# Optimization experiments

Hardware: AMD Instinct MI355X
Metric: run time of the kernel (lower is better)

The kernel has to match this reference:

```python
import jax, jax.numpy as jnp
import numpy as np

N_HEAD = 16
D_MODEL = 1024
D_HEAD = D_MODEL // N_HEAD
B, T = 2, 2048


def setup_inputs() -> dict:
    key = jax.random.key(0)
    k1, k2, k3 = jax.random.split(key, 3)
    x = jax.random.normal(k1, (B, T, D_MODEL), dtype=jnp.float32)
    w_attn = jax.random.normal(k2, (3 * D_MODEL, D_MODEL), dtype=jnp.float32) * (D_MODEL ** -0.5)
    w_proj = jax.random.normal(k3, (D_MODEL, D_MODEL), dtype=jnp.float32) * (D_MODEL ** -0.5)
    return {"x": x, "w_attn": w_attn, "w_proj": w_proj}


def _rms_norm(x):
    eps = jnp.asarray(jnp.finfo(x.dtype).eps, x.dtype)
    var = jnp.mean(jnp.square(x), axis=-1, keepdims=True)
    return x * jax.lax.rsqrt(var + eps)


def _rotate_half(x):
    x1, x2 = jnp.split(x, 2, axis=-1)
    return jnp.concatenate((-x2, x1), axis=-1)


def reference(x, w_attn, w_proj):
    Bx, Tx, C = x.shape
    qkv = jnp.einsum('btc,fc->btf', x, w_attn)  # [B,T,3C]
    q, k, v = jnp.split(qkv, 3, axis=-1)
    # [B, H, T, Dh]
    q = q.reshape(Bx, Tx, N_HEAD, D_HEAD).transpose(0, 2, 1, 3)
    k = k.reshape(Bx, Tx, N_HEAD, D_HEAD).transpose(0, 2, 1, 3)
    v = v.reshape(Bx, Tx, N_HEAD, D_HEAD).transpose(0, 2, 1, 3)
    # QK RMSNorm (no learned weight)
    q = _rms_norm(q)
    k = _rms_norm(k)
    # Rotary embedding over full d_head: freqs tiled twice
    inv_freq = 1.0 / (10000.0 ** (jnp.arange(0, D_HEAD, 2, dtype=jnp.float32) / D_HEAD))
    t = jnp.arange(Tx, dtype=jnp.float32)
    freqs = jnp.einsum('i,j->ij', t, inv_freq)  # [T, Dh/2]
    emb = jnp.concatenate((freqs, freqs), axis=-1)  # [T, Dh]
    cos = jnp.cos(emb)[None, None, :, :]
    sin = jnp.sin(emb)[None, None, :, :]
    q = q * cos + _rotate_half(q) * sin
    k = k * cos + _rotate_half(k) * sin
    # Causal SDPA
    scale = D_HEAD ** -0.5
    scores = jnp.einsum('bhqd,bhkd->bhqk', q, k) * scale
    causal = jnp.tril(jnp.ones((Tx, Tx), dtype=bool))
    scores = jnp.where(causal[None, None], scores, jnp.asarray(-jnp.inf, scores.dtype))
    attn = jax.nn.softmax(scores, axis=-1)
    y = jnp.einsum('bhqk,bhkd->bhqd', attn, v)
    y = y.transpose(0, 2, 1, 3).reshape(Bx, Tx, C)
    return jnp.einsum('btc,oc->bto', y, w_proj)
```

## Files before the change

kernel.cpp:

```cpp
#include <hip/hip_runtime.h>
#include <cstdint>
#include <cstddef>


typedef short bf16x8 __attribute__((ext_vector_type(8)));
typedef float floatx4 __attribute__((ext_vector_type(4)));
typedef unsigned short ushortx8 __attribute__((ext_vector_type(8)));
typedef unsigned short ushortx4 __attribute__((ext_vector_type(4)));

#define DEVI __device__ __forceinline__

DEVI float bf2f(unsigned short u) {
    unsigned int x = ((unsigned int)u) << 16;
    return __builtin_bit_cast(float, x);
}
DEVI unsigned short f2bf(float f) {
    unsigned int u = __builtin_bit_cast(unsigned int, f);
    u += 0x7fffu + ((u >> 16) & 1u);
    return (unsigned short)(u >> 16);
}

DEVI void glds16(const unsigned short* g, unsigned short* l) {
    __builtin_amdgcn_global_load_lds(
        (const __attribute__((address_space(1))) unsigned int*)g,
        (__attribute__((address_space(3))) unsigned int*)l, 16, 0, 0);
}

DEVI void cast8(unsigned short* dst, const float* src) {
    floatx4 a = *(const floatx4*)src;
    floatx4 b = *(const floatx4*)(src + 4);
    ushortx8 o;
    o[0] = f2bf(a[0]); o[1] = f2bf(a[1]); o[2] = f2bf(a[2]); o[3] = f2bf(a[3]);
    o[4] = f2bf(b[0]); o[5] = f2bf(b[1]); o[6] = f2bf(b[2]); o[7] = f2bf(b[3]);
    *(ushortx8*)dst = o;
}

__global__ __launch_bounds__(256)
void cast_inputs(const float* __restrict__ x, const float* __restrict__ wa,
                 const float* __restrict__ wp,
                 unsigned short* __restrict__ xb, unsigned short* __restrict__ wab,
                 unsigned short* __restrict__ wpb)
{
    size_t g = (size_t)blockIdx.x * 256 + threadIdx.x;
    size_t stride = (size_t)gridDim.x * 256;
    for (size_t i = g; i < (4194304 / 8); i += stride) cast8(xb  + i * 8, x  + i * 8);
    for (size_t i = g; i < (3145728 / 8); i += stride) cast8(wab + i * 8, wa + i * 8);
    for (size_t i = g; i < (1048576 / 8); i += stride) cast8(wpb + i * 8, wp + i * 8);
}

template <bool QKV_SPLIT>
__global__ __launch_bounds__(256)
void gemm_bt(const unsigned short* __restrict__ A, const unsigned short* __restrict__ B,
             unsigned short* __restrict__ Cqk, float* __restrict__ Cf,
             unsigned short* __restrict__ Vt, int M, int N, int K)
{
    __shared__ __align__(16) unsigned short As[128 * 32];
    __shared__ __align__(16) unsigned short Bs[128 * 32];

    const int tid  = threadIdx.x;
    const int lane = tid & 63;
    const int w    = tid >> 6;
    const int wm   = w >> 1, wn = w & 1;
    const int quad = lane >> 4;
    const int lm   = lane & 15;
    const int m0 = blockIdx.y * 128;
    const int n0 = blockIdx.x * 128;
    const int sr = lane >> 2;
    const int sc = (lane & 3) * 8;

    floatx4 acc[4][4] = {};

    for (int k0 = 0; k0 < K; k0 += 32) {
        __syncthreads();
        #pragma unroll
        for (int i = 0; i < 2; ++i) {
            int r = w * 32 + i * 16;
            glds16(&A[(size_t)(m0 + r + sr) * K + k0 + sc], &As[r * 32]);
            glds16(&B[(size_t)(n0 + r + sr) * K + k0 + sc], &Bs[r * 32]);
        }
        __syncthreads();

        bf16x8 a[4];
        #pragma unroll
        for (int i = 0; i < 4; ++i)
            a[i] = *(const bf16x8*)&As[(wm * 64 + i * 16 + lm) * 32 + quad * 8];
        #pragma unroll
        for (int j = 0; j < 4; ++j) {
            bf16x8 b = *(const bf16x8*)&Bs[(wn * 64 + j * 16 + lm) * 32 + quad * 8];
            #pragma unroll
            for (int i = 0; i < 4; ++i)
                acc[i][j] = __builtin_amdgcn_mfma_f32_16x16x32_bf16(a[i], b, acc[i][j], 0, 0, 0);
        }
    }

    #pragma unroll
    for (int i = 0; i < 4; ++i) {
        #pragma unroll
        for (int j = 0; j < 4; ++j) {
            int col = n0 + wn * 64 + j * 16 + lm;
            #pragma unroll
            for (int r = 0; r < 4; ++r) {
                int row = m0 + wm * 64 + i * 16 + quad * 4 + r;
                if constexpr (QKV_SPLIT) {
                    unsigned short v = f2bf(acc[i][j][r]);
                    if (col < 2048) {
                        Cqk[(size_t)row * 2048 + col] = v;
                    } else {
                        int bq = row >> 11, t = row & 2047;
                        Vt[((size_t)(bq * 1024 + (col - 2048))) * 2048 + t] = v;
                    }
                } else {
                    Cf[(size_t)row * N + col] = acc[i][j][r];
                }
            }
        }
    }
}

__global__ __launch_bounds__(256)
void rmsnorm_rope(unsigned short* __restrict__ qk)
{
    int gw   = (blockIdx.x * 256 + threadIdx.x) >> 6;
    int lane = threadIdx.x & 63;
    int h = gw & 15;
    int t = (gw >> 4) & 2047;
    int b = gw >> 15;

    size_t base = ((size_t)(b * 2048 + t)) * 2048 + h * 64 + lane;
    float q = bf2f(qk[base]);
    float k = bf2f(qk[base + 1024]);

    float sq = q * q, sk = k * k;
    #pragma unroll
    for (int off = 32; off >= 1; off >>= 1) {
        sq += __shfl_xor(sq, off, 64);
        sk += __shfl_xor(sk, off, 64);
    }
    const float eps = 1.1920929e-07f;
    q *= rsqrtf(sq * (1.0f / 64.0f) + eps);
    k *= rsqrtf(sk * (1.0f / 64.0f) + eps);

    int i = lane & 31;
    float ang = (float)t * expf(-(float)i * 0.28782313662425572f);
    float c = cosf(ang), s = sinf(ang);
    float qp = __shfl_xor(q, 32, 64);
    float kp = __shfl_xor(k, 32, 64);
    float sgn = (lane < 32) ? -1.0f : 1.0f;
    float qo = q * c + sgn * qp * s;
    float ko = k * c + sgn * kp * s;

    qk[base]        = f2bf(qo);
    qk[base + 1024] = f2bf(ko);
}

__global__ __launch_bounds__(256)
void attention(const unsigned short* __restrict__ qk,
               const unsigned short* __restrict__ Vt,
               unsigned short* __restrict__ Y)
{
    constexpr int LD = 72;
    __shared__ __align__(16) unsigned short QPs[64 * LD];
    __shared__ __align__(16) unsigned short Ks [64 * LD];
    __shared__ __align__(16) unsigned short Vs [64 * LD];

    const int tid  = threadIdx.x;
    const int lane = tid & 63;
    const int w    = tid >> 6;
    const int quad = lane >> 4;
    const int lm   = lane & 15;

    const int bh = blockIdx.x;
    const int qt = 31 - blockIdx.y;
    const int b  = bh >> 4, h = bh & 15;
    const int q0 = qt * 64;
    const int qrow = q0 + w * 16 + lm;

    #pragma unroll
    for (int i = 0; i < 2; ++i) {
        int c = i * 256 + tid, row = c >> 3, col = (c & 7) * 8;
        *(ushortx8*)&QPs[row * LD + col] =
            *(const ushortx8*)&qk[((size_t)(b * 2048 + q0 + row)) * 2048 + h * 64 + col];
    }

    ushortx8 kreg[2], vreg[2];
    #pragma unroll
    for (int i = 0; i < 2; ++i) {
        int c = i * 256 + tid, row = c >> 3, col = (c & 7) * 8;
        kreg[i] = *(const ushortx8*)&qk[((size_t)(b * 2048 + row)) * 2048 + 1024 + h * 64 + col];
        vreg[i] = *(const ushortx8*)&Vt[((size_t)(bh * 64 + row)) * 2048 + col];
    }

    floatx4 o[4] = {};
    float lsum = 0.0f;
    bf16x8 qf[2];
    const float c1 = 0.125f * 1.44269504f;
    const float c2 = 8.0f   * 1.44269504f;

    for (int kt = 0; kt <= qt; ++kt) {
        const int k0 = kt * 64;
        __syncthreads();
        #pragma unroll
        for (int i = 0; i < 2; ++i) {
            int c = i * 256 + tid, row = c >> 3, col = (c & 7) * 8;
            *(ushortx8*)&Ks[row * LD + col] = kreg[i];
            *(ushortx8*)&Vs[row * LD + col] = vreg[i];
        }
        __syncthreads();

        if (kt == 0) {
            #pragma unroll
            for (int kk = 0; kk < 2; ++kk)
                qf[kk] = *(const bf16x8*)&QPs[(w * 16 + lm) * LD + kk * 32 + quad * 8];
        }
        if (kt < qt) {
            const int kn = k0 + 64;
            #pragma unroll
            for (int i = 0; i < 2; ++i) {
                int c = i * 256 + tid, row = c >> 3, col = (c & 7) * 8;
                kreg[i] = *(const ushortx8*)&qk[((size_t)(b * 2048 + kn + row)) * 2048 + 1024 + h * 64 + col];
                vreg[i] = *(const ushortx8*)&Vt[((size_t)(bh * 64 + row)) * 2048 + kn + col];
            }
        }

        floatx4 sa[4] = {};
        #pragma unroll
        for (int kk = 0; kk < 2; ++kk) {
            #pragma unroll
            for (int j = 0; j < 4; ++j) {
                bf16x8 kf = *(const bf16x8*)&Ks[(j * 16 + lm) * LD + kk * 32 + quad * 8];
                sa[j] = __builtin_amdgcn_mfma_f32_16x16x32_bf16(kf, qf[kk], sa[j], 0, 0, 0);
            }
        }

        const bool dg = (kt == qt);
        #pragma unroll
        for (int j = 0; j < 4; ++j) {
            int kbase = k0 + j * 16 + quad * 4;
            ushortx4 pk;
            #pragma unroll
            for (int r = 0; r < 4; ++r) {
                float p = exp2f(sa[j][r] * c1 - c2);
                if (dg && (kbase + r) > qrow) p = 0.0f;
                lsum += p;
                pk[r] = f2bf(p);
            }
            *(ushortx4*)&QPs[(w * 16 + lm) * LD + j * 16 + quad * 4] = pk;
        }

        #pragma unroll
        for (int kk = 0; kk < 2; ++kk) {
            bf16x8 pf = *(const bf16x8*)&QPs[(w * 16 + lm) * LD + kk * 32 + quad * 8];
            #pragma unroll
            for (int j = 0; j < 4; ++j) {
                bf16x8 vf = *(const bf16x8*)&Vs[(j * 16 + lm) * LD + kk * 32 + quad * 8];
                o[j] = __builtin_amdgcn_mfma_f32_16x16x32_bf16(pf, vf, o[j], 0, 0, 0);
            }
        }
    }

    float lt = lsum;
    lt += __shfl_xor(lt, 16, 64);
    lt += __shfl_xor(lt, 32, 64);
    float rv = 1.0f / lt;
    float rinv[4];
    #pragma unroll
    for (int r = 0; r < 4; ++r)
        rinv[r] = __shfl(rv, (quad << 4) + quad * 4 + r, 64);

    #pragma unroll
    for (int j = 0; j < 4; ++j) {
        int colg = h * 64 + j * 16 + lm;
        #pragma unroll
        for (int r = 0; r < 4; ++r) {
            int rowg = q0 + w * 16 + quad * 4 + r;
            Y[((size_t)(b * 2048 + rowg)) * 1024 + colg] = f2bf(o[j][r] * rinv[r]);
        }
    }
}

extern "C" void kernel_launch(void* const* d_in, const int* in_sizes, int n_in,
                              void* d_out, int out_size, void* d_ws, size_t ws_size,
                              hipStream_t stream)
{
    const float* x      = (const float*)d_in[0];
    const float* w_attn = (const float*)d_in[1];
    const float* w_proj = (const float*)d_in[2];
    float* out = (float*)d_out;

    unsigned short* qkbuf = (unsigned short*)d_ws;
    unsigned short* Vtb   = qkbuf + (size_t)4096 * 2048;
    unsigned short* y     = Vtb   + (size_t)32 * 64 * 2048;
    unsigned short* wpb   = y     + (size_t)4096 * 1024;
    unsigned short* xb  = (unsigned short*)d_out;
    unsigned short* wab = xb + (size_t)4096 * 1024;

    dim3 blk(256);
    cast_inputs<<<dim3(1024), blk, 0, stream>>>(x, w_attn, w_proj, xb, wab, wpb);
    gemm_bt<true>
        <<<dim3(24, 32), blk, 0, stream>>>(xb, wab, qkbuf, nullptr, Vtb, 4096, 3072, 1024);
    rmsnorm_rope<<<dim3(16384), blk, 0, stream>>>(qkbuf);
    attention<<<dim3(32, 32), blk, 0, stream>>>(qkbuf, Vtb, y);
    gemm_bt<false>
        <<<dim3(8, 32), blk, 0, stream>>>(y, wpb, nullptr, out, nullptr, 4096, 1024, 1024);
}
```

Baseline: 212.0 us.

## Double-buffer K/V register prefetch two tiles ahead and pack bf16 with perm

K/V tiles are now prefetched into a two-deep register ring, loading the tile two iterations ahead instead of one, so global-load latency has more compute to hide behind. The __syncthreads pairs are replaced by an inline-asm waitcnt lgkmcnt(0)+s_barrier. P conversion to bf16 now uses round-half-up plus a byte permute that packs two values per instruction, instead of round-to-nearest-even per element. The cost is more VGPRs for the extra prefetch buffers, which may lower occupancy, plus a slightly different bf16 rounding.

Result: slower. 719.7 us (+239.5%).

```diff
diff --git a/kernel.cpp b/kernel.cpp
--- a/kernel.cpp
+++ b/kernel.cpp
@@ -6,7 +6,7 @@
 typedef short bf16x8 __attribute__((ext_vector_type(8)));
 typedef float floatx4 __attribute__((ext_vector_type(4)));
 typedef unsigned short ushortx8 __attribute__((ext_vector_type(8)));
-typedef unsigned short ushortx4 __attribute__((ext_vector_type(4)));
+typedef unsigned int uintx2 __attribute__((ext_vector_type(2)));
 
 #define DEVI __device__ __forceinline__
 
@@ -18,6 +18,14 @@
     unsigned int u = __builtin_bit_cast(unsigned int, f);
     u += 0x7fffu + ((u >> 16) & 1u);
     return (unsigned short)(u >> 16);
+}
+DEVI unsigned int pkbf2(float a, float b) {
+    unsigned int ua = __builtin_bit_cast(unsigned int, a) + 0x8000u;
+    unsigned int ub = __builtin_bit_cast(unsigned int, b) + 0x8000u;
+    return __builtin_amdgcn_perm(ub, ua, 0x07060302);
+}
+DEVI void barrier_lgkm() {
+    asm volatile("s_waitcnt lgkmcnt(0)\ns_barrier" ::: "memory");
 }
 
 DEVI void glds16(const unsigned short* g, unsigned short* l) {
@@ -175,6 +183,11 @@
     const int q0 = qt * 64;
     const int qrow = q0 + w * 16 + lm;
 
+    const int pr0 = tid >> 3,        pc = (tid & 7) * 8;
+    const int pr1 = (256 + tid) >> 3;
+    const unsigned short* kbase = qk + (size_t)b * 2048 * 2048 + 1024 + h * 64;
+    const unsigned short* vbase = Vt + (size_t)bh * 64 * 2048;
+
     #pragma unroll
     for (int i = 0; i < 2; ++i) {
         int c = i * 256 + tid, row = c >> 3, col = (c & 7) * 8;
@@ -182,12 +195,17 @@
             *(const ushortx8*)&qk[((size_t)(b * 2048 + q0 + row)) * 2048 + h * 64 + col];
     }
 
-    ushortx8 kreg[2], vreg[2];
-    #pragma unroll
-    for (int i = 0; i < 2; ++i) {
-        int c = i * 256 + tid, row = c >> 3, col = (c & 7) * 8;
-        kreg[i] = *(const ushortx8*)&qk[((size_t)(b * 2048 + row)) * 2048 + 1024 + h * 64 + col];
-        vreg[i] = *(const ushortx8*)&Vt[((size_t)(bh * 64 + row)) * 2048 + col];
+    ushortx8 kreg[2][2], vreg[2][2];
+    {
+        kreg[0][0] = *(const ushortx8*)&kbase[(size_t)pr0 * 2048 + pc];
+        kreg[0][1] = *(const ushortx8*)&kbase[(size_t)pr1 * 2048 + pc];
+        vreg[0][0] = *(const ushortx8*)&vbase[(size_t)pr0 * 2048 + pc];
+        vreg[0][1] = *(const ushortx8*)&vbase[(size_t)pr1 * 2048 + pc];
+        int t1 = (qt >= 1) ? 64 : 0;
+        kreg[1][0] = *(const ushortx8*)&kbase[(size_t)(t1 + pr0) * 2048 + pc];
+        kreg[1][1] = *(const ushortx8*)&kbase[(size_t)(t1 + pr1) * 2048 + pc];
+        vreg[1][0] = *(const ushortx8*)&vbase[(size_t)pr0 * 2048 + t1 + pc];
+        vreg[1][1] = *(const ushortx8*)&vbase[(size_t)pr1 * 2048 + t1 + pc];
     }
 
     floatx4 o[4] = {};
@@ -198,28 +216,25 @@
 
     for (int kt = 0; kt <= qt; ++kt) {
         const int k0 = kt * 64;
-        __syncthreads();
-        #pragma unroll
-        for (int i = 0; i < 2; ++i) {
-            int c = i * 256 + tid, row = c >> 3, col = (c & 7) * 8;
-            *(ushortx8*)&Ks[row * LD + col] = kreg[i];
-            *(ushortx8*)&Vs[row * LD + col] = vreg[i];
-        }
-        __syncthreads();
+        const int cur = kt & 1;
+        barrier_lgkm();
+        *(ushortx8*)&Ks[pr0 * LD + pc] = kreg[cur][0];
+        *(ushortx8*)&Ks[pr1 * LD + pc] = kreg[cur][1];
+        *(ushortx8*)&Vs[pr0 * LD + pc] = vreg[cur][0];
+        *(ushortx8*)&Vs[pr1 * LD + pc] = vreg[cur][1];
+        barrier_lgkm();
 
         if (kt == 0) {
             #pragma unroll
             for (int kk = 0; kk < 2; ++kk)
                 qf[kk] = *(const bf16x8*)&QPs[(w * 16 + lm) * LD + kk * 32 + quad * 8];
         }
-        if (kt < qt) {
-            const int kn = k0 + 64;
-            #pragma unroll
-            for (int i = 0; i < 2; ++i) {
-                int c = i * 256 + tid, row = c >> 3, col = (c & 7) * 8;
-                kreg[i] = *(const ushortx8*)&qk[((size_t)(b * 2048 + kn + row)) * 2048 + 1024 + h * 64 + col];
-                vreg[i] = *(const ushortx8*)&Vt[((size_t)(bh * 64 + row)) * 2048 + kn + col];
-            }
+        if (kt + 2 <= qt) {
+            const int kn = k0 + 128;
+            kreg[cur][0] = *(const ushortx8*)&kbase[(size_t)(kn + pr0) * 2048 + pc];
+            kreg[cur][1] = *(const ushortx8*)&kbase[(size_t)(kn + pr1) * 2048 + pc];
+            vreg[cur][0] = *(const ushortx8*)&vbase[(size_t)pr0 * 2048 + kn + pc];
+            vreg[cur][1] = *(const ushortx8*)&vbase[(size_t)pr1 * 2048 + kn + pc];
         }
 
         floatx4 sa[4] = {};
@@ -235,16 +250,22 @@
         const bool dg = (kt == qt);
         #pragma unroll
         for (int j = 0; j < 4; ++j) {
-            int kbase = k0 + j * 16 + quad * 4;
-            ushortx4 pk;
-            #pragma unroll
-            for (int r = 0; r < 4; ++r) {
-                float p = exp2f(sa[j][r] * c1 - c2);
-                if (dg && (kbase + r) > qrow) p = 0.0f;
-                lsum += p;
-                pk[r] = f2bf(p);
+            int kb = k0 + j * 16 + quad * 4;
+            float p0 = exp2f(sa[j][0] * c1 - c2);
+            float p1 = exp2f(sa[j][1] * c1 - c2);
+            float p2 = exp2f(sa[j][2] * c1 - c2);
+            float p3 = exp2f(sa[j][3] * c1 - c2);
+            if (dg) {
+                if (kb + 0 > qrow) p0 = 0.0f;
+                if (kb + 1 > qrow) p1 = 0.0f;
+                if (kb + 2 > qrow) p2 = 0.0f;
+                if (kb + 3 > qrow) p3 = 0.0f;
             }
-            *(ushortx4*)&QPs[(w * 16 + lm) * LD + j * 16 + quad * 4] = pk;
+            lsum += (p0 + p1) + (p2 + p3);
+            uintx2 pk;
+            pk[0] = pkbf2(p0, p1);
+            pk[1] = pkbf2(p2, p3);
+            *(uintx2*)&QPs[(w * 16 + lm) * LD + j * 16 + quad * 4] = pk;
         }
 
         #pragma unroll
```

## Pair causal query tiles per attention block and narrow output-projection GEMM tiles

Applied to the files above, without the earlier changes.

The attention kernel now launches half as many blocks. Each block processes two query tiles, qt and 31-qt, so every block does the same total causal work instead of the triangular imbalance. The output-projection GEMM is templated to a 128x64 tile with a 4x1 wave layout, doubling its grid from 256 to 512 blocks to fill more CUs. In exchange, attention gets fewer concurrent blocks and runs longer serial loops per block, and the narrower GEMM tile reduces reuse of the A operand.

Result: no change. 209.5 us (-1.2%).

```diff
diff --git a/kernel.cpp b/kernel.cpp
--- a/kernel.cpp
+++ b/kernel.cpp
@@ -48,27 +48,31 @@
     for (size_t i = g; i < (1048576 / 8); i += stride) cast8(wpb + i * 8, wp + i * 8);
 }
 
-template <bool QKV_SPLIT>
+template <bool QKV_SPLIT, int BN>
 __global__ __launch_bounds__(256)
 void gemm_bt(const unsigned short* __restrict__ A, const unsigned short* __restrict__ B,
              unsigned short* __restrict__ Cqk, float* __restrict__ Cf,
              unsigned short* __restrict__ Vt, int M, int N, int K)
 {
+    constexpr int WCOLS = (BN == 128) ? 2 : 1;
+    constexpr int WROWS = 4 / WCOLS;
+    constexpr int MI    = 128 / (16 * WROWS);
+
     __shared__ __align__(16) unsigned short As[128 * 32];
-    __shared__ __align__(16) unsigned short Bs[128 * 32];
+    __shared__ __align__(16) unsigned short Bs[BN * 32];
 
     const int tid  = threadIdx.x;
     const int lane = tid & 63;
     const int w    = tid >> 6;
-    const int wm   = w >> 1, wn = w & 1;
+    const int wm   = w / WCOLS, wn = w % WCOLS;
     const int quad = lane >> 4;
     const int lm   = lane & 15;
     const int m0 = blockIdx.y * 128;
-    const int n0 = blockIdx.x * 128;
+    const int n0 = blockIdx.x * BN;
     const int sr = lane >> 2;
     const int sc = (lane & 3) * 8;
 
-    floatx4 acc[4][4] = {};
+    floatx4 acc[MI][4] = {};
 
     for (int k0 = 0; k0 < K; k0 += 32) {
         __syncthreads();
@@ -76,31 +80,35 @@
         for (int i = 0; i < 2; ++i) {
             int r = w * 32 + i * 16;
             glds16(&A[(size_t)(m0 + r + sr) * K + k0 + sc], &As[r * 32]);
+        }
+        #pragma unroll
+        for (int i = 0; i < BN / 64; ++i) {
+            int r = w * (BN / 4) + i * 16;
             glds16(&B[(size_t)(n0 + r + sr) * K + k0 + sc], &Bs[r * 32]);
         }
         __syncthreads();
 
-        bf16x8 a[4];
-        #pragma unroll
-        for (int i = 0; i < 4; ++i)
-            a[i] = *(const bf16x8*)&As[(wm * 64 + i * 16 + lm) * 32 + quad * 8];
+        bf16x8 a[MI];
+        #pragma unroll
+        for (int i = 0; i < MI; ++i)
+            a[i] = *(const bf16x8*)&As[(wm * (16 * MI) + i * 16 + lm) * 32 + quad * 8];
         #pragma unroll
         for (int j = 0; j < 4; ++j) {
             bf16x8 b = *(const bf16x8*)&Bs[(wn * 64 + j * 16 + lm) * 32 + quad * 8];
             #pragma unroll
-            for (int i = 0; i < 4; ++i)
+            for (int i = 0; i < MI; ++i)
                 acc[i][j] = __builtin_amdgcn_mfma_f32_16x16x32_bf16(a[i], b, acc[i][j], 0, 0, 0);
         }
     }
 
     #pragma unroll
-    for (int i = 0; i < 4; ++i) {
+    for (int i = 0; i < MI; ++i) {
         #pragma unroll
         for (int j = 0; j < 4; ++j) {
             int col = n0 + wn * 64 + j * 16 + lm;
             #pragma unroll
             for (int r = 0; r < 4; ++r) {
-                int row = m0 + wm * 64 + i * 16 + quad * 4 + r;
+                int row = m0 + wm * (16 * MI) + i * 16 + quad * 4 + r;
                 if constexpr (QKV_SPLIT) {
                     unsigned short v = f2bf(acc[i][j][r]);
                     if (col < 2048) {
@@ -170,110 +178,119 @@
     const int lm   = lane & 15;
 
     const int bh = blockIdx.x;
-    const int qt = 31 - blockIdx.y;
     const int b  = bh >> 4, h = bh & 15;
-    const int q0 = qt * 64;
-    const int qrow = q0 + w * 16 + lm;
+
+    const unsigned short* kbase = qk + (size_t)b * 2048 * 2048 + 1024 + h * 64;
+    const unsigned short* vbase = Vt + (size_t)bh * 64 * 2048;
 
     #pragma unroll
-    for (int i = 0; i < 2; ++i) {
-        int c = i * 256 + tid, row = c >> 3, col = (c & 7) * 8;
-        *(ushortx8*)&QPs[row * LD + col] =
-            *(const ushortx8*)&qk[((size_t)(b * 2048 + q0 + row)) * 2048 + h * 64 + col];
-    }
-
-    ushortx8 kreg[2], vreg[2];
-    #pragma unroll
-    for (int i = 0; i < 2; ++i) {
-        int c = i * 256 + tid, row = c >> 3, col = (c & 7) * 8;
-        kreg[i] = *(const ushortx8*)&qk[((size_t)(b * 2048 + row)) * 2048 + 1024 + h * 64 + col];
-        vreg[i] = *(const ushortx8*)&Vt[((size_t)(bh * 64 + row)) * 2048 + col];
-    }
-
-    floatx4 o[4] = {};
-    float lsum = 0.0f;
-    bf16x8 qf[2];
-    const float c1 = 0.125f * 1.44269504f;
-    const float c2 = 8.0f   * 1.44269504f;
-
-    for (int kt = 0; kt <= qt; ++kt) {
-        const int k0 = kt * 64;
-        __syncthreads();
+    for (int sel = 0; sel < 2; ++sel) {
+        const int qt = sel ? (int)blockIdx.y : 31 - (int)blockIdx.y;
+        const int q0 = qt * 64;
+        const int qrow = q0 + w * 16 + lm;
+
+        if (sel) __syncthreads();
+
         #pragma unroll
         for (int i = 0; i < 2; ++i) {
             int c = i * 256 + tid, row = c >> 3, col = (c & 7) * 8;
-            *(ushortx8*)&Ks[row * LD + col] = kreg[i];
-            *(ushortx8*)&Vs[row * LD + col] = vreg[i];
-        }
-        __syncthreads();
-
-        if (kt == 0) {
-            #pragma unroll
-            for (int kk = 0; kk < 2; ++kk)
-                qf[kk] = *(const bf16x8*)&QPs[(w * 16 + lm) * LD + kk * 32 + quad * 8];
-        }
-        if (kt < qt) {
-            const int kn = k0 + 64;
+            *(ushortx8*)&QPs[row * LD + col] =
+                *(const ushortx8*)&qk[((size_t)(b * 2048 + q0 + row)) * 2048 + h * 64 + col];
+        }
+
+        ushortx8 kreg[2], vreg[2];
+        #pragma unroll
+        for (int i = 0; i < 2; ++i) {
+            int c = i * 256 + tid, row = c >> 3, col = (c & 7) * 8;
+            kreg[i] = *(const ushortx8*)&kbase[(size_t)row * 2048 + col];
+            vreg[i] = *(const ushortx8*)&vbase[(size_t)row * 2048 + col];
+        }
+
+        floatx4 o[4] = {};
+        float lsum = 0.0f;
+        bf16x8 qf[2];
+        const float c1 = 0.125f * 1.44269504f;
+        const float c2 = 8.0f   * 1.44269504f;
+
+        for (int kt = 0; kt <= qt; ++kt) {
+            const int k0 = kt * 64;
+            __syncthreads();
             #pragma unroll
             for (int i = 0; i < 2; ++i) {
                 int c = i * 256 + tid, row = c >> 3, col = (c & 7) * 8;
-                kreg[i] = *(const ushortx8*)&qk[((size_t)(b * 2048 + kn + row)) * 2048 + 1024 + h * 64 + col];
-                vreg[i] = *(const ushortx8*)&Vt[((size_t)(bh * 64 + row)) * 2048 + kn + col];
-            }
-        }
-
-        floatx4 sa[4] = {};
-        #pragma unroll
-        for (int kk = 0; kk < 2; ++kk) {
+                *(ushortx8*)&Ks[row * LD + col] = kreg[i];
+                *(ushortx8*)&Vs[row * LD + col] = vreg[i];
+            }
+            __syncthreads();
+
+            if (kt == 0) {
+                #pragma unroll
+                for (int kk = 0; kk < 2; ++kk)
+                    qf[kk] = *(const bf16x8*)&QPs[(w * 16 + lm) * LD + kk * 32 + quad * 8];
+            }
+            if (kt < qt) {
+                const int kn = k0 + 64;
+                #pragma unroll
+                for (int i = 0; i < 2; ++i) {
+                    int c = i * 256 + tid, row = c >> 3, col = (c & 7) * 8;
+                    kreg[i] = *(const ushortx8*)&kbase[(size_t)(kn + row) * 2048 + col];
+                    vreg[i] = *(const ushortx8*)&vbase[(size_t)row * 2048 + kn + col];
+                }
+            }
+
+            floatx4 sa[4] = {};
+            #pragma unroll
+            for (int kk = 0; kk < 2; ++kk) {
+                #pragma unroll
+                for (int j = 0; j < 4; ++j) {
+                    bf16x8 kf = *(const bf16x8*)&Ks[(j * 16 + lm) * LD + kk * 32 + quad * 8];
+                    sa[j] = __builtin_amdgcn_mfma_f32_16x16x32_bf16(kf, qf[kk], sa[j], 0, 0, 0);
+                }
+            }
+
+            const bool dg = (kt == qt);
             #pragma unroll
             for (int j = 0; j < 4; ++j) {
-                bf16x8 kf = *(const bf16x8*)&Ks[(j * 16 + lm) * LD + kk * 32 + quad * 8];
-                sa[j] = __builtin_amdgcn_mfma_f32_16x16x32_bf16(kf, qf[kk], sa[j], 0, 0, 0);
-            }
-        }
-
-        const bool dg = (kt == qt);
+                int kb = k0 + j * 16 + quad * 4;
+                ushortx4 pk;
+                #pragma unroll
+                for (int r = 0; r < 4; ++r) {
+                    float p = exp2f(sa[j][r] * c1 - c2);
+                    if (dg && (kb + r) > qrow) p = 0.0f;
+                    lsum += p;
+                    pk[r] = f2bf(p);
+                }
+                *(ushortx4*)&QPs[(w * 16 + lm) * LD + j * 16 + quad * 4] = pk;
+            }
+
+            #pragma unroll
+            for (int kk = 0; kk < 2; ++kk) {
+                bf16x8 pf = *(const bf16x8*)&QPs[(w * 16 + lm) * LD + kk * 32 + quad * 8];
+                #pragma unroll
+                for (int j = 0; j < 4; ++j) {
+                    bf16x8 vf = *(const bf16x8*)&Vs[(j * 16 + lm) * LD + kk * 32 + quad * 8];
+                    o[j] = __builtin_amdgcn_mfma_f32_16x16x32_bf16(pf, vf, o[j], 0, 0, 0);
+                }
+            }
+        }
+
+        float lt = lsum;
+        lt += __shfl_xor(lt, 16, 64);
+        lt += __shfl_xor(lt, 32, 64);
+        float rv = 1.0f / lt;
+        float rinv[4];
+        #pragma unroll
+        for (int r = 0; r < 4; ++r)
+            rinv[r] = __shfl(rv, (quad << 4) + quad * 4 + r, 64);
+
         #pragma unroll
         for (int j = 0; j < 4; ++j) {
-            int kbase = k0 + j * 16 + quad * 4;
-            ushortx4 pk;
+            int colg = h * 64 + j * 16 + lm;
             #pragma unroll
             for (int r = 0; r < 4; ++r) {
-                float p = exp2f(sa[j][r] * c1 - c2);
-                if (dg && (kbase + r) > qrow) p = 0.0f;
-                lsum += p;
-                pk[r] = f2bf(p);
-            }
-            *(ushortx4*)&QPs[(w * 16 + lm) * LD + j * 16 + quad * 4] = pk;
-        }
-
-        #pragma unroll
-        for (int kk = 0; kk < 2; ++kk) {
-            bf16x8 pf = *(const bf16x8*)&QPs[(w * 16 + lm) * LD + kk * 32 + quad * 8];
-            #pragma unroll
-            for (int j = 0; j < 4; ++j) {
-                bf16x8 vf = *(const bf16x8*)&Vs[(j * 16 + lm) * LD + kk * 32 + quad * 8];
-                o[j] = __builtin_amdgcn_mfma_f32_16x16x32_bf16(pf, vf, o[j], 0, 0, 0);
-            }
-        }
-    }
-
-    float lt = lsum;
-    lt += __shfl_xor(lt, 16, 64);
-    lt += __shfl_xor(lt, 32, 64);
-    float rv = 1.0f / lt;
-    float rinv[4];
-    #pragma unroll
-    for (int r = 0; r < 4; ++r)
-        rinv[r] = __shfl(rv, (quad << 4) + quad * 4 + r, 64);
-
-    #pragma unroll
-    for (int j = 0; j < 4; ++j) {
-        int colg = h * 64 + j * 16 + lm;
-        #pragma unroll
-        for (int r = 0; r < 4; ++r) {
-            int rowg = q0 + w * 16 + quad * 4 + r;
-            Y[((size_t)(b * 2048 + rowg)) * 1024 + colg] = f2bf(o[j][r] * rinv[r]);
+                int rowg = q0 + w * 16 + quad * 4 + r;
+                Y[((size_t)(b * 2048 + rowg)) * 1024 + colg] = f2bf(o[j][r] * rinv[r]);
+            }
         }
     }
 }
@@ -296,10 +313,10 @@
 
     dim3 blk(256);
     cast_inputs<<<dim3(1024), blk, 0, stream>>>(x, w_attn, w_proj, xb, wab, wpb);
-    gemm_bt<true>
+    gemm_bt<true, 128>
         <<<dim3(24, 32), blk, 0, stream>>>(xb, wab, qkbuf, nullptr, Vtb, 4096, 3072, 1024);
     rmsnorm_rope<<<dim3(16384), blk, 0, stream>>>(qkbuf);
-    attention<<<dim3(32, 32), blk, 0, stream>>>(qkbuf, Vtb, y);
-    gemm_bt<false>
-        <<<dim3(8, 32), blk, 0, stream>>>(y, wpb, nullptr, out, nullptr, 4096, 1024, 1024);
-}
+    attention<<<dim3(32, 16), blk, 0, stream>>>(qkbuf, Vtb, y);
+    gemm_bt<false, 64>
+        <<<dim3(16, 32), blk, 0, stream>>>(y, wpb, nullptr, out, nullptr, 4096, 1024, 1024);
+}
```
